# Optimization experiments

Measured on AMD Instinct MI355X. Metric: run time of the kernel, lower is better.

Reference implementation:

```python
import jax, jax.numpy as jnp
import numpy as np

NEG_SLOPE = 0.01


def reference(feat_src, feat_dst, src, dst, attn_l, attn_r):
    # feat_src: [Ns, D], feat_dst: [Nd, D], src/dst: [E] int, attn_*: [1, D]
    n_dst = feat_dst.shape[0]
    el = (feat_src * attn_l).sum(axis=-1)  # [Ns]
    er = (feat_dst * attn_r).sum(axis=-1)  # [Nd]
    e = el[src] + er[dst]                  # [E]
    e = jnp.where(e >= 0, e, NEG_SLOPE * e)  # leaky_relu
    # edge softmax over incoming edges of each destination node
    m = jax.ops.segment_max(e, dst, num_segments=n_dst)  # [Nd]
    m = jnp.where(jnp.isfinite(m), m, 0.0)  # guard empty segments
    a = jnp.exp(e - m[dst])                 # [E]
    denom = jax.ops.segment_sum(a, dst, num_segments=n_dst)  # [Nd]
    denom = jnp.where(denom > 0, denom, 1.0)
    a = a / denom[dst]
    # weighted scatter-sum of source features: [E, D] messages -> [Nd, D]
    msg = feat_src[src] * a[:, None]
    out = jax.ops.segment_sum(msg, dst, num_segments=n_dst)
    return out


def setup_inputs() -> dict:
    key = jax.random.key(0)
    k1, k2, k3, k4, k5, k6 = jax.random.split(key, 6)
    Ns, Nd, E, D = 100000, 100000, 1600000, 128
    return {
        "feat_src": jax.random.normal(k1, (Ns, D), dtype=jnp.float32),
        "feat_dst": jax.random.normal(k2, (Nd, D), dtype=jnp.float32),
        "src": jax.random.randint(k3, (E,), 0, Ns, dtype=jnp.int32),
        "dst": jax.random.randint(k4, (E,), 0, Nd, dtype=jnp.int32),
        "attn_l": jax.random.normal(k5, (1, D), dtype=jnp.float32) * 0.1,
        "attn_r": jax.random.normal(k6, (1, D), dtype=jnp.float32) * 0.1,
    }
```

## Files before the change

### kernel.cpp

```cpp
#include <hip/hip_runtime.h>
#include <hip/hip_bf16.h>
#include <math.h>

#define D 128
#define AGG_THREADS 128
#define CHUNK 512
#define BSHIFT 8
#define MAXB 1024
#define MAXWG 1024
#define PCHUNK 4096
#define PE 16
#define EBUF_CAP 5120
#define PR 8192

__device__ __forceinline__ unsigned short f2bf(float f) {
    union { float f; unsigned int u; } c; c.f = f;
    unsigned int u = c.u;
    unsigned int r = (u + 0x7FFFu + ((u >> 16) & 1u)) >> 16;
    return (unsigned short)r;
}
__device__ __forceinline__ void unpack2(unsigned int w, float& lo, float& hi) {
    union { unsigned int u; float f; } c;
    c.u = w << 16;          lo = c.f;
    c.u = w & 0xFFFF0000u;  hi = c.f;
}

__global__ void prep_kernel(const float* __restrict__ feat_src,
                            const float* __restrict__ feat_dst,
                            const float* __restrict__ attn_l,
                            const float* __restrict__ attn_r,
                            float* __restrict__ el, float* __restrict__ er,
                            unsigned short* __restrict__ feat_bf, int store_bf,
                            int Ns, int Nd) {
    int half = threadIdx.x >> 5;
    int lane = threadIdx.x & 31;
    int node = blockIdx.x * 8 + half;
    if (node >= Ns + Nd) return;
    bool is_src = node < Ns;
    const float* feat = is_src ? feat_src + (size_t)node * D
                               : feat_dst + (size_t)(node - Ns) * D;
    const float* attn = is_src ? attn_l : attn_r;
    float4 a = ((const float4*)attn)[lane];
    float4 v = ((const float4*)feat)[lane];
    if (is_src && store_bf) {
        ushort4 h; h.x = f2bf(v.x); h.y = f2bf(v.y); h.z = f2bf(v.z); h.w = f2bf(v.w);
        ((ushort4*)(feat_bf + (size_t)node * D))[lane] = h;
    }
    float s = v.x * a.x + v.y * a.y + v.z * a.z + v.w * a.w;
    #pragma unroll
    for (int off = 16; off > 0; off >>= 1)
        s += __shfl_xor(s, off, 64);
    if (lane == 0) {
        if (is_src) el[node] = s;
        else        er[node - Ns] = s;
    }
}

__global__ void partition_kernel(const int* __restrict__ src, const int* __restrict__ dst,
                                 int E, int nbk,
                                 uint2* __restrict__ bins,
                                 int* __restrict__ cnt_tab, int* __restrict__ loc_tab) {
    __shared__ int hist[MAXB];
    __shared__ int lstart[MAXB];
    __shared__ int cursor[MAXB];
    __shared__ uint2 sbuf[PCHUNK];
    int w = blockIdx.x, tid = threadIdx.x;
    int e0 = w * PCHUNK;
    int e1 = min(E, e0 + PCHUNK);
    int n = e1 - e0;

    for (int i = tid; i < nbk; i += 256) hist[i] = 0;
    __syncthreads();

    int es[PE], ed[PE];
    #pragma unroll
    for (int k = 0; k < PE; ++k) {
        int idx = e0 + k * 256 + tid;
        if (idx < e1) {
            es[k] = src[idx];
            ed[k] = dst[idx];
            atomicAdd(&hist[ed[k] >> BSHIFT], 1);
        }
    }
    __syncthreads();

    if (tid < 64) {
        int carry = 0;
        for (int c = 0; c < nbk; c += 64) {
            int i = c + tid;
            int v = (i < nbk) ? hist[i] : 0;
            int x = v;
            #pragma unroll
            for (int off = 1; off < 64; off <<= 1) {
                int t = __shfl_up(x, off, 64);
                if (tid >= off) x += t;
            }
            if (i < nbk) lstart[i] = x - v + carry;
            carry += __shfl(x, 63, 64);
        }
    }
    __syncthreads();

    for (int i = tid; i < nbk; i += 256) {
        cnt_tab[(size_t)w * nbk + i] = hist[i];
        loc_tab[(size_t)w * nbk + i] = lstart[i];
        cursor[i] = 0;
    }
    __syncthreads();

    #pragma unroll
    for (int k = 0; k < PE; ++k) {
        int idx = e0 + k * 256 + tid;
        if (idx < e1) {
            int b = ed[k] >> BSHIFT;
            int r = lstart[b] + atomicAdd(&cursor[b], 1);
            sbuf[r] = make_uint2((unsigned)es[k], (unsigned)ed[k]);
        }
    }
    __syncthreads();

    uint2* obase = bins + (size_t)w * PCHUNK;
    for (int t = tid; t < n; t += 256) obase[t] = sbuf[t];
}

__global__ void bucket_kernel(const uint2* __restrict__ bins,
                              const int* __restrict__ cnt_tab, const int* __restrict__ loc_tab,
                              int nbk, int nwg,
                              int* __restrict__ counts, int* __restrict__ offs,
                              int* __restrict__ perm, int Nd) {
    __shared__ uint2 ebuf[EBUF_CAP];
    __shared__ int wcnt[MAXWG];
    __shared__ int wdst[MAXWG];
    __shared__ int sbase[MAXWG];
    __shared__ int cnt256[256];
    __shared__ int off256[256];
    __shared__ int cur256[256];
    __shared__ int tile[256];
    __shared__ int total_sh;

    int b = blockIdx.x, tid = threadIdx.x;
    int base = b << BSHIFT;

    for (int i = tid; i < nwg; i += 256) wcnt[i] = cnt_tab[(size_t)i * nbk + b];
    __syncthreads();
    if (tid < 64) {
        int carry = 0;
        for (int c = 0; c < nwg; c += 64) {
            int i = c + tid;
            int v = (i < nwg) ? wcnt[i] : 0;
            int x = v;
            #pragma unroll
            for (int off = 1; off < 64; off <<= 1) {
                int t = __shfl_up(x, off, 64);
                if (tid >= off) x += t;
            }
            if (i < nwg) wdst[i] = x - v + carry;
            carry += __shfl(x, 63, 64);
        }
        if (tid == 0) total_sh = carry;
    }
    cnt256[tid] = 0;
    cur256[tid] = 0;
    __syncthreads();
    int n = total_sh;
    bool fits = (n <= EBUF_CAP);

    if (fits) {
        for (int w = tid; w < nwg; w += 256)
            sbase[w] = w * PCHUNK + loc_tab[(size_t)w * nbk + b] - wdst[w];
        __syncthreads();
        for (int t = tid; t < n; t += 256) {
            int lo = 0, hi = nwg - 1;
            while (lo < hi) {
                int mid = (lo + hi + 1) >> 1;
                if (wdst[mid] <= t) lo = mid; else hi = mid - 1;
            }
            uint2 e = bins[(size_t)(sbase[lo] + t)];
            ebuf[t] = e;
            atomicAdd(&cnt256[(int)e.y - base], 1);
        }
    } else {
        for (int w = tid; w < nwg; w += 256) {
            int c = wcnt[w];
            const uint2* sp = bins + (size_t)w * PCHUNK + loc_tab[(size_t)w * nbk + b];
            for (int k = 0; k < c; ++k)
                atomicAdd(&cnt256[(int)sp[k].y - base], 1);
        }
        __syncthreads();
    }
    __syncthreads();

    int v = cnt256[tid];
    tile[tid] = v;
    __syncthreads();
    for (int off = 1; off < 256; off <<= 1) {
        int t = (tid >= off) ? tile[tid - off] : 0;
        __syncthreads();
        tile[tid] += t;
        __syncthreads();
    }
    int myoff = tile[tid] - v;
    off256[tid] = myoff;
    int i = base + tid;
    if (i < Nd) {
        int c = v;
        if (myoff + c > PR) c = max(0, PR - myoff);
        counts[i] = c;
        offs[i]   = myoff;
    }
    __syncthreads();

    size_t rbase = (size_t)b * PR;
    if (fits) {
        for (int t = tid; t < n; t += 256) {
            uint2 e = ebuf[t];
            int d = (int)e.y - base;
            int r = atomicAdd(&cur256[d], 1);
            int slot = off256[d] + r;
            if (slot < PR) perm[rbase + slot] = (int)e.x;
        }
    } else {
        for (int w = tid; w < nwg; w += 256) {
            int c = wcnt[w];
            const uint2* sp = bins + (size_t)w * PCHUNK + loc_tab[(size_t)w * nbk + b];
            for (int k = 0; k < c; ++k) {
                uint2 e = sp[k];
                int d = (int)e.y - base;
                int r = atomicAdd(&cur256[d], 1);
                int slot = off256[d] + r;
                if (slot < PR) perm[rbase + slot] = (int)e.x;
            }
        }
    }
}

__device__ __forceinline__ float block_max128(float v, float* red, int tid) {
    #pragma unroll
    for (int off = 32; off > 0; off >>= 1)
        v = fmaxf(v, __shfl_down(v, off, 64));
    __syncthreads();
    if ((tid & 63) == 0) red[tid >> 6] = v;
    __syncthreads();
    return fmaxf(red[0], red[1]);
}
__device__ __forceinline__ float block_sum128(float v, float* red, int tid) {
    #pragma unroll
    for (int off = 32; off > 0; off >>= 1)
        v += __shfl_down(v, off, 64);
    __syncthreads();
    if ((tid & 63) == 0) red[tid >> 6] = v;
    __syncthreads();
    return red[0] + red[1];
}

__global__ void gat_aggregate_wave_kernel(const unsigned short* __restrict__ feat_bf,
                                          const float* __restrict__ el,
                                          const float* __restrict__ er,
                                          const int* __restrict__ offs,
                                          const int* __restrict__ counts,
                                          const int* __restrict__ perm,
                                          float* __restrict__ out, int Nd) {
    int wid  = threadIdx.x >> 6;
    int lane = threadIdx.x & 63;
    int j = blockIdx.x * 4 + wid;
    if (j >= Nd) return;
    int cnt = counts[j];
    size_t orow = (size_t)j * D;
    if (cnt == 0) {
        ((float2*)(out + orow))[lane] = make_float2(0.0f, 0.0f);
        return;
    }
    size_t beg = (size_t)(j >> BSHIFT) * PR + (size_t)offs[j];
    float erj = er[j];
    int sg = lane >> 4, u = lane & 15;
    const unsigned short* fb = feat_bf + (size_t)u * 8;
    float acc[8];
    #pragma unroll
    for (int k = 0; k < 8; ++k) acc[k] = 0.0f;

    if (cnt <= 64) {
        int s = 0; float e = -INFINITY;
        if (lane < cnt) {
            s = perm[beg + lane];
            float t = el[s] + erj;
            e = (t >= 0.0f) ? t : 0.01f * t;
        }
        float m = e;
        #pragma unroll
        for (int off = 32; off > 0; off >>= 1)
            m = fmaxf(m, __shfl_xor(m, off, 64));
        float a = (lane < cnt) ? __expf(e - m) : 0.0f;
        float den = a;
        #pragma unroll
        for (int off = 32; off > 0; off >>= 1)
            den += __shfl_xor(den, off, 64);
        a *= (1.0f / den);
        int nit = (cnt + 3) >> 2;
        for (int it = 0; it < nit; ++it) {
            int t = sg + (it << 2);
            int tt = (t < cnt) ? t : 0;
            float w = __shfl(a, tt, 64);
            int st  = __shfl(s, tt, 64);
            if (t < cnt) {
                uint4 v = *(const uint4*)(fb + (size_t)st * D);
                float f[8];
                unpack2(v.x, f[0], f[1]); unpack2(v.y, f[2], f[3]);
                unpack2(v.z, f[4], f[5]); unpack2(v.w, f[6], f[7]);
                #pragma unroll
                for (int k = 0; k < 8; ++k) acc[k] += w * f[k];
            }
        }
    } else {
        float lmax = -INFINITY;
        for (int t = lane; t < cnt; t += 64) {
            int s = perm[beg + t];
            float e = el[s] + erj;
            e = (e >= 0.0f) ? e : 0.01f * e;
            lmax = fmaxf(lmax, e);
        }
        float m = lmax;
        #pragma unroll
        for (int off = 32; off > 0; off >>= 1)
            m = fmaxf(m, __shfl_xor(m, off, 64));
        float lsum = 0.0f;
        for (int t = lane; t < cnt; t += 64) {
            int s = perm[beg + t];
            float e = el[s] + erj;
            e = (e >= 0.0f) ? e : 0.01f * e;
            lsum += __expf(e - m);
        }
        #pragma unroll
        for (int off = 32; off > 0; off >>= 1)
            lsum += __shfl_xor(lsum, off, 64);
        float inv = 1.0f / lsum;
        for (int bb = 0; bb < cnt; bb += 64) {
            int nn = min(64, cnt - bb);
            int s = 0; float a = 0.0f;
            if (lane < nn) {
                s = perm[beg + bb + lane];
                float e = el[s] + erj;
                e = (e >= 0.0f) ? e : 0.01f * e;
                a = __expf(e - m) * inv;
            }
            int nit = (nn + 3) >> 2;
            for (int it = 0; it < nit; ++it) {
                int t = sg + (it << 2);
                int tt = (t < nn) ? t : 0;
                float w = __shfl(a, tt, 64);
                int st  = __shfl(s, tt, 64);
                if (t < nn) {
                    uint4 v = *(const uint4*)(fb + (size_t)st * D);
                    float f[8];
                    unpack2(v.x, f[0], f[1]); unpack2(v.y, f[2], f[3]);
                    unpack2(v.z, f[4], f[5]); unpack2(v.w, f[6], f[7]);
                    #pragma unroll
                    for (int k = 0; k < 8; ++k) acc[k] += w * f[k];
                }
            }
        }
    }
    #pragma unroll
    for (int k = 0; k < 8; ++k) {
        acc[k] += __shfl_xor(acc[k], 16, 64);
        acc[k] += __shfl_xor(acc[k], 32, 64);
    }
    if (sg == 0) {
        float* op = out + orow + (size_t)u * 8;
        ((float4*)op)[0] = make_float4(acc[0], acc[1], acc[2], acc[3]);
        ((float4*)op)[1] = make_float4(acc[4], acc[5], acc[6], acc[7]);
    }
}

__global__ void hist_kernel(const int* __restrict__ dst, int E, int* __restrict__ counts) {
    int stride = gridDim.x * blockDim.x;
    for (int k = blockIdx.x * blockDim.x + threadIdx.x; k < E; k += stride)
        atomicAdd(&counts[dst[k]], 1);
}
__global__ void scan1_kernel(const int* __restrict__ counts, int* __restrict__ offsets,
                             int* __restrict__ blockSums, int N) {
    __shared__ int tile[256];
    int tid = threadIdx.x;
    int i = blockIdx.x * 256 + tid;
    int v = (i < N) ? counts[i] : 0;
    tile[tid] = v;
    __syncthreads();
    for (int off = 1; off < 256; off <<= 1) {
        int t = (tid >= off) ? tile[tid - off] : 0;
        __syncthreads();
        tile[tid] += t;
        __syncthreads();
    }
    int incl = tile[tid];
    if (i < N) offsets[i] = incl - v;
    if (tid == 255) blockSums[blockIdx.x] = incl;
}
__global__ void scan2_kernel(int* __restrict__ bs, int nb) {
    __shared__ int tile[256];
    int tid = threadIdx.x;
    int carry = 0;
    for (int base = 0; base < nb; base += 256) {
        int i = base + tid;
        int v = (i < nb) ? bs[i] : 0;
        __syncthreads();
        tile[tid] = v;
        __syncthreads();
        for (int off = 1; off < 256; off <<= 1) {
            int t = (tid >= off) ? tile[tid - off] : 0;
            __syncthreads();
            tile[tid] += t;
            __syncthreads();
        }
        int incl = tile[tid];
        if (i < nb) bs[i] = incl - v + carry;
        carry += tile[255];
    }
}
__global__ void fill_kernel(const int* __restrict__ src, const int* __restrict__ dst, int E,
                            const int* __restrict__ offsets, const int* __restrict__ bsum,
                            int* __restrict__ cursor, int* __restrict__ perm_src) {
    int stride = gridDim.x * blockDim.x;
    for (int k = blockIdx.x * blockDim.x + threadIdx.x; k < E; k += stride) {
        int j = dst[k];
        int p = offsets[j] + bsum[j >> BSHIFT] + atomicAdd(&cursor[j], 1);
        perm_src[p] = src[k];
    }
}
__global__ void gat_aggregate_f32_kernel(const float* __restrict__ feat_src,
                                         const float* __restrict__ el,
                                         const float* __restrict__ er,
                                         const int* __restrict__ offsets,
                                         const int* __restrict__ bsum,
                                         const int* __restrict__ counts,
                                         const int* __restrict__ perm_src,
                                         float* __restrict__ out, int Nd) {
    __shared__ float w_sh[CHUNK];
    __shared__ int   s_sh[CHUNK];
    __shared__ float red[2];
    int j = blockIdx.x;
    int tid = threadIdx.x;
    int cnt = counts[j];
    size_t orow = (size_t)j * D;
    if (cnt == 0) { out[orow + tid] = 0.0f; return; }
    int beg = offsets[j] + bsum[j >> BSHIFT];
    float erj = er[j];
    float acc = 0.0f;
    float inv;
    if (cnt <= CHUNK) {
        float lmax = -INFINITY;
        for (int t = tid; t < cnt; t += AGG_THREADS) {
            int s = perm_src[beg + t];
            float e = el[s] + erj;
            e = (e >= 0.0f) ? e : 0.01f * e;
            s_sh[t] = s; w_sh[t] = e;
            lmax = fmaxf(lmax, e);
        }
        float m = block_max128(lmax, red, tid);
        float lsum = 0.0f;
        for (int t = tid; t < cnt; t += AGG_THREADS) {
            float a = __expf(w_sh[t] - m);
            w_sh[t] = a; lsum += a;
        }
        float den = block_sum128(lsum, red, tid);
        inv = 1.0f / den;
        __syncthreads();
        for (int t = 0; t < cnt; ++t)
            acc += feat_src[(size_t)s_sh[t] * D + tid] * w_sh[t];
    } else {
        float lmax = -INFINITY;
        for (int t = tid; t < cnt; t += AGG_THREADS) {
            int s = perm_src[beg + t];
            float e = el[s] + erj;
            e = (e >= 0.0f) ? e : 0.01f * e;
            lmax = fmaxf(lmax, e);
        }
        float m = block_max128(lmax, red, tid);
        float lsum = 0.0f;
        for (int t = tid; t < cnt; t += AGG_THREADS) {
            int s = perm_src[beg + t];
            float e = el[s] + erj;
            e = (e >= 0.0f) ? e : 0.01f * e;
            lsum += __expf(e - m);
        }
        float den = block_sum128(lsum, red, tid);
        inv = 1.0f / den;
        for (int bb = 0; bb < cnt; bb += CHUNK) {
            int n = min(CHUNK, cnt - bb);
            __syncthreads();
            for (int t = tid; t < n; t += AGG_THREADS) {
                int s = perm_src[beg + bb + t];
                float e = el[s] + erj;
                e = (e >= 0.0f) ? e : 0.01f * e;
                s_sh[t] = s;
                w_sh[t] = __expf(e - m);
            }
            __syncthreads();
            for (int t = 0; t < n; ++t)
                acc += feat_src[(size_t)s_sh[t] * D + tid] * w_sh[t];
        }
    }
    out[orow + tid] = acc * inv;
}

extern "C" void kernel_launch(void* const* d_in, const int* in_sizes, int n_in,
                              void* d_out, int out_size, void* d_ws, size_t ws_size,
                              hipStream_t stream) {
    const float* feat_src = (const float*)d_in[0];
    const float* feat_dst = (const float*)d_in[1];
    const int*   src      = (const int*)d_in[2];
    const int*   dst      = (const int*)d_in[3];
    const float* attn_l   = (const float*)d_in[4];
    const float* attn_r   = (const float*)d_in[5];
    float* out = (float*)d_out;

    int Ns = in_sizes[0] / D;
    int Nd = in_sizes[1] / D;
    int E  = in_sizes[2];
    int NBK = (Nd + (1 << BSHIFT) - 1) >> BSHIFT;
    int NWG = (E + PCHUNK - 1) / PCHUNK;

    char* p = (char*)d_ws;
    auto carve = [&](size_t bytes) { void* r = (void*)p; p += (bytes + 255) & ~(size_t)255; return r; };
    float* el      = (float*)carve((size_t)Ns * 4);
    float* er      = (float*)carve((size_t)Nd * 4);
    int*   counts  = (int*)carve((size_t)Nd * 4);
    int*   offs    = (int*)carve((size_t)Nd * 4);
    int*   gcursor = (int*)carve((size_t)Nd * 4);
    int*   bsums   = (int*)carve((size_t)NBK * 4);
    int*   cnt_tab = (int*)carve((size_t)NWG * NBK * 4);
    int*   loc_tab = (int*)carve((size_t)NWG * NBK * 4);
    int*   perm    = (int*)carve((size_t)NBK * PR * 4);
    uint2* bins    = (uint2*)carve((size_t)NWG * PCHUNK * 8);
    size_t used    = (size_t)(p - (char*)d_ws);
    size_t bf_bytes = (size_t)Ns * D * 2;
    unsigned short* feat_bf = (unsigned short*)carve(bf_bytes);

    int fast = (NBK <= MAXB && NWG <= MAXWG &&
                used + bf_bytes + 256 <= ws_size) ? 1 : 0;

    int total = Ns + Nd;
    if (fast) {
        prep_kernel<<<(total + 7) / 8, 256, 0, stream>>>(feat_src, feat_dst, attn_l, attn_r,
                                                         el, er, feat_bf, 1, Ns, Nd);
        partition_kernel<<<NWG, 256, 0, stream>>>(src, dst, E, NBK, bins, cnt_tab, loc_tab);
        bucket_kernel<<<NBK, 256, 0, stream>>>(bins, cnt_tab, loc_tab, NBK, NWG,
                                               counts, offs, perm, Nd);
        gat_aggregate_wave_kernel<<<(Nd + 3) / 4, 256, 0, stream>>>(feat_bf, el, er, offs,
                                                                    counts, perm, out, Nd);
    } else {
        hipMemsetAsync(counts, 0, (size_t)Nd * 4, stream);
        hipMemsetAsync(gcursor, 0, (size_t)Nd * 4, stream);
        prep_kernel<<<(total + 7) / 8, 256, 0, stream>>>(feat_src, feat_dst, attn_l, attn_r,
                                                         el, er, nullptr, 0, Ns, Nd);
        hist_kernel<<<2048, 256, 0, stream>>>(dst, E, counts);
        scan1_kernel<<<NBK, 256, 0, stream>>>(counts, offs, bsums, Nd);
        scan2_kernel<<<1, 256, 0, stream>>>(bsums, NBK);
        fill_kernel<<<2048, 256, 0, stream>>>(src, dst, E, offs, bsums, gcursor, perm);
        gat_aggregate_f32_kernel<<<Nd, AGG_THREADS, 0, stream>>>(feat_src, el, er, offs,
                                                                 bsums, counts, perm, out, Nd);
    }
}
```

Baseline: 265.1 us.

## Replace two-pass bucketed partition with atomic histogram, scan and fill CSR build

Removes the partition and bucket kernels that built a per-bucket, capped-size edge permutation. The destination histogram is now folded into the prep kernel as a grid-stride atomic loop, followed by a global two-level scan and an atomic fill kernel that produces an exact CSR permutation. The aggregation kernel now indexes it through offsets plus block sums. This drops the per-bucket PR cap and the intermediate bins buffer. In exchange it relies on global atomics with random scatter in the fill step, adds more launches and memsets, and loses the locality of the bucketed layout.

```diff
diff --git a/kernel.cpp b/kernel.cpp
--- a/kernel.cpp
+++ b/kernel.cpp
@@ -6,12 +6,6 @@
 #define AGG_THREADS 128
 #define CHUNK 512
 #define BSHIFT 8
-#define MAXB 1024
-#define MAXWG 1024
-#define PCHUNK 4096
-#define PE 16
-#define EBUF_CAP 5120
-#define PR 8192
 
 __device__ __forceinline__ unsigned short f2bf(float f) {
     union { float f; unsigned int u; } c; c.f = f;
@@ -29,9 +23,16 @@
                             const float* __restrict__ feat_dst,
                             const float* __restrict__ attn_l,
                             const float* __restrict__ attn_r,
+                            const int* __restrict__ dst, int E,
+                            int* __restrict__ counts,
                             float* __restrict__ el, float* __restrict__ er,
                             unsigned short* __restrict__ feat_bf, int store_bf,
                             int Ns, int Nd) {
+    int gid = blockIdx.x * 256 + threadIdx.x;
+    int gstride = gridDim.x * 256;
+    for (int k = gid; k < E; k += gstride)
+        atomicAdd(&counts[dst[k]], 1);
+
     int half = threadIdx.x >> 5;
     int lane = threadIdx.x & 31;
     int node = blockIdx.x * 8 + half;
@@ -56,141 +57,12 @@
     }
 }
 
-__global__ void partition_kernel(const int* __restrict__ src, const int* __restrict__ dst,
-                                 int E, int nbk,
-                                 uint2* __restrict__ bins,
-                                 int* __restrict__ cnt_tab, int* __restrict__ loc_tab) {
-    __shared__ int hist[MAXB];
-    __shared__ int lstart[MAXB];
-    __shared__ int cursor[MAXB];
-    __shared__ uint2 sbuf[PCHUNK];
-    int w = blockIdx.x, tid = threadIdx.x;
-    int e0 = w * PCHUNK;
-    int e1 = min(E, e0 + PCHUNK);
-    int n = e1 - e0;
-
-    for (int i = tid; i < nbk; i += 256) hist[i] = 0;
-    __syncthreads();
-
-    int es[PE], ed[PE];
-    #pragma unroll
-    for (int k = 0; k < PE; ++k) {
-        int idx = e0 + k * 256 + tid;
-        if (idx < e1) {
-            es[k] = src[idx];
-            ed[k] = dst[idx];
-            atomicAdd(&hist[ed[k] >> BSHIFT], 1);
-        }
-    }
-    __syncthreads();
-
-    if (tid < 64) {
-        int carry = 0;
-        for (int c = 0; c < nbk; c += 64) {
-            int i = c + tid;
-            int v = (i < nbk) ? hist[i] : 0;
-            int x = v;
-            #pragma unroll
-            for (int off = 1; off < 64; off <<= 1) {
-                int t = __shfl_up(x, off, 64);
-                if (tid >= off) x += t;
-            }
-            if (i < nbk) lstart[i] = x - v + carry;
-            carry += __shfl(x, 63, 64);
-        }
-    }
-    __syncthreads();
-
-    for (int i = tid; i < nbk; i += 256) {
-        cnt_tab[(size_t)w * nbk + i] = hist[i];
-        loc_tab[(size_t)w * nbk + i] = lstart[i];
-        cursor[i] = 0;
-    }
-    __syncthreads();
-
-    #pragma unroll
-    for (int k = 0; k < PE; ++k) {
-        int idx = e0 + k * 256 + tid;
-        if (idx < e1) {
-            int b = ed[k] >> BSHIFT;
-            int r = lstart[b] + atomicAdd(&cursor[b], 1);
-            sbuf[r] = make_uint2((unsigned)es[k], (unsigned)ed[k]);
-        }
-    }
-    __syncthreads();
-
-    uint2* obase = bins + (size_t)w * PCHUNK;
-    for (int t = tid; t < n; t += 256) obase[t] = sbuf[t];
-}
-
-__global__ void bucket_kernel(const uint2* __restrict__ bins,
-                              const int* __restrict__ cnt_tab, const int* __restrict__ loc_tab,
-                              int nbk, int nwg,
-                              int* __restrict__ counts, int* __restrict__ offs,
-                              int* __restrict__ perm, int Nd) {
-    __shared__ uint2 ebuf[EBUF_CAP];
-    __shared__ int wcnt[MAXWG];
-    __shared__ int wdst[MAXWG];
-    __shared__ int sbase[MAXWG];
-    __shared__ int cnt256[256];
-    __shared__ int off256[256];
-    __shared__ int cur256[256];
+__global__ void scan1_kernel(const int* __restrict__ counts, int* __restrict__ offsets,
+                             int* __restrict__ blockSums, int N) {
     __shared__ int tile[256];
-    __shared__ int total_sh;
-
-    int b = blockIdx.x, tid = threadIdx.x;
-    int base = b << BSHIFT;
-
-    for (int i = tid; i < nwg; i += 256) wcnt[i] = cnt_tab[(size_t)i * nbk + b];
-    __syncthreads();
-    if (tid < 64) {
-        int carry = 0;
-        for (int c = 0; c < nwg; c += 64) {
-            int i = c + tid;
-            int v = (i < nwg) ? wcnt[i] : 0;
-            int x = v;
-            #pragma unroll
-            for (int off = 1; off < 64; off <<= 1) {
-                int t = __shfl_up(x, off, 64);
-                if (tid >= off) x += t;
-            }
-            if (i < nwg) wdst[i] = x - v + carry;
-            carry += __shfl(x, 63, 64);
-        }
-        if (tid == 0) total_sh = carry;
-    }
-    cnt256[tid] = 0;
-    cur256[tid] = 0;
-    __syncthreads();
-    int n = total_sh;
-    bool fits = (n <= EBUF_CAP);
-
-    if (fits) {
-        for (int w = tid; w < nwg; w += 256)
-            sbase[w] = w * PCHUNK + loc_tab[(size_t)w * nbk + b] - wdst[w];
-        __syncthreads();
-        for (int t = tid; t < n; t += 256) {
-            int lo = 0, hi = nwg - 1;
-            while (lo < hi) {
-                int mid = (lo + hi + 1) >> 1;
-                if (wdst[mid] <= t) lo = mid; else hi = mid - 1;
-            }
-            uint2 e = bins[(size_t)(sbase[lo] + t)];
-            ebuf[t] = e;
-            atomicAdd(&cnt256[(int)e.y - base], 1);
-        }
-    } else {
-        for (int w = tid; w < nwg; w += 256) {
-            int c = wcnt[w];
-            const uint2* sp = bins + (size_t)w * PCHUNK + loc_tab[(size_t)w * nbk + b];
-            for (int k = 0; k < c; ++k)
-                atomicAdd(&cnt256[(int)sp[k].y - base], 1);
-        }
-        __syncthreads();
-    }
-    __syncthreads();
-
-    int v = cnt256[tid];
+    int tid = threadIdx.x;
+    int i = blockIdx.x * 256 + tid;
+    int v = (i < N) ? counts[i] : 0;
     tile[tid] = v;
     __syncthreads();
     for (int off = 1; off < 256; off <<= 1) {
@@ -199,38 +71,40 @@
         tile[tid] += t;
         __syncthreads();
     }
-    int myoff = tile[tid] - v;
-    off256[tid] = myoff;
-    int i = base + tid;
-    if (i < Nd) {
-        int c = v;
-        if (myoff + c > PR) c = max(0, PR - myoff);
-        counts[i] = c;
-        offs[i]   = myoff;
-    }
-    __syncthreads();
-
-    size_t rbase = (size_t)b * PR;
-    if (fits) {
-        for (int t = tid; t < n; t += 256) {
-            uint2 e = ebuf[t];
-            int d = (int)e.y - base;
-            int r = atomicAdd(&cur256[d], 1);
-            int slot = off256[d] + r;
-            if (slot < PR) perm[rbase + slot] = (int)e.x;
-        }
-    } else {
-        for (int w = tid; w < nwg; w += 256) {
-            int c = wcnt[w];
-            const uint2* sp = bins + (size_t)w * PCHUNK + loc_tab[(size_t)w * nbk + b];
-            for (int k = 0; k < c; ++k) {
-                uint2 e = sp[k];
-                int d = (int)e.y - base;
-                int r = atomicAdd(&cur256[d], 1);
-                int slot = off256[d] + r;
-                if (slot < PR) perm[rbase + slot] = (int)e.x;
-            }
-        }
+    int incl = tile[tid];
+    if (i < N) offsets[i] = incl - v;
+    if (tid == 255) blockSums[blockIdx.x] = incl;
+}
+__global__ void scan2_kernel(int* __restrict__ bs, int nb) {
+    __shared__ int tile[256];
+    int tid = threadIdx.x;
+    int carry = 0;
+    for (int base = 0; base < nb; base += 256) {
+        int i = base + tid;
+        int v = (i < nb) ? bs[i] : 0;
+        __syncthreads();
+        tile[tid] = v;
+        __syncthreads();
+        for (int off = 1; off < 256; off <<= 1) {
+            int t = (tid >= off) ? tile[tid - off] : 0;
+            __syncthreads();
+            tile[tid] += t;
+            __syncthreads();
+        }
+        int incl = tile[tid];
+        if (i < nb) bs[i] = incl - v + carry;
+        carry += tile[255];
+    }
+}
+
+__global__ void fill_kernel(const int* __restrict__ src, const int* __restrict__ dst, int E,
+                            const int* __restrict__ offsets, const int* __restrict__ bsum,
+                            int* __restrict__ cursor, int* __restrict__ perm_src) {
+    int stride = gridDim.x * blockDim.x;
+    for (int k = blockIdx.x * blockDim.x + threadIdx.x; k < E; k += stride) {
+        int j = dst[k];
+        int p = offsets[j] + bsum[j >> BSHIFT] + atomicAdd(&cursor[j], 1);
+        perm_src[p] = src[k];
     }
 }
 
@@ -257,6 +131,7 @@
                                           const float* __restrict__ el,
                                           const float* __restrict__ er,
                                           const int* __restrict__ offs,
+                                          const int* __restrict__ bsum,
                                           const int* __restrict__ counts,
                                           const int* __restrict__ perm,
                                           float* __restrict__ out, int Nd) {
@@ -270,7 +145,7 @@
         ((float2*)(out + orow))[lane] = make_float2(0.0f, 0.0f);
         return;
     }
-    size_t beg = (size_t)(j >> BSHIFT) * PR + (size_t)offs[j];
+    size_t beg = (size_t)offs[j] + (size_t)bsum[j >> BSHIFT];
     float erj = er[j];
     int sg = lane >> 4, u = lane & 15;
     const unsigned short* fb = feat_bf + (size_t)u * 8;
@@ -371,60 +246,6 @@
     }
 }
 
-__global__ void hist_kernel(const int* __restrict__ dst, int E, int* __restrict__ counts) {
-    int stride = gridDim.x * blockDim.x;
-    for (int k = blockIdx.x * blockDim.x + threadIdx.x; k < E; k += stride)
-        atomicAdd(&counts[dst[k]], 1);
-}
-__global__ void scan1_kernel(const int* __restrict__ counts, int* __restrict__ offsets,
-                             int* __restrict__ blockSums, int N) {
-    __shared__ int tile[256];
-    int tid = threadIdx.x;
-    int i = blockIdx.x * 256 + tid;
-    int v = (i < N) ? counts[i] : 0;
-    tile[tid] = v;
-    __syncthreads();
-    for (int off = 1; off < 256; off <<= 1) {
-        int t = (tid >= off) ? tile[tid - off] : 0;
-        __syncthreads();
-        tile[tid] += t;
-        __syncthreads();
-    }
-    int incl = tile[tid];
-    if (i < N) offsets[i] = incl - v;
-    if (tid == 255) blockSums[blockIdx.x] = incl;
-}
-__global__ void scan2_kernel(int* __restrict__ bs, int nb) {
-    __shared__ int tile[256];
-    int tid = threadIdx.x;
-    int carry = 0;
-    for (int base = 0; base < nb; base += 256) {
-        int i = base + tid;
-        int v = (i < nb) ? bs[i] : 0;
-        __syncthreads();
-        tile[tid] = v;
-        __syncthreads();
-        for (int off = 1; off < 256; off <<= 1) {
-            int t = (tid >= off) ? tile[tid - off] : 0;
-            __syncthreads();
-            tile[tid] += t;
-            __syncthreads();
-        }
-        int incl = tile[tid];
-        if (i < nb) bs[i] = incl - v + carry;
-        carry += tile[255];
-    }
-}
-__global__ void fill_kernel(const int* __restrict__ src, const int* __restrict__ dst, int E,
-                            const int* __restrict__ offsets, const int* __restrict__ bsum,
-                            int* __restrict__ cursor, int* __restrict__ perm_src) {
-    int stride = gridDim.x * blockDim.x;
-    for (int k = blockIdx.x * blockDim.x + threadIdx.x; k < E; k += stride) {
-        int j = dst[k];
-        int p = offsets[j] + bsum[j >> BSHIFT] + atomicAdd(&cursor[j], 1);
-        perm_src[p] = src[k];
-    }
-}
 __global__ void gat_aggregate_f32_kernel(const float* __restrict__ feat_src,
                                          const float* __restrict__ el,
                                          const float* __restrict__ er,
@@ -516,7 +337,6 @@
     int Nd = in_sizes[1] / D;
     int E  = in_sizes[2];
     int NBK = (Nd + (1 << BSHIFT) - 1) >> BSHIFT;
-    int NWG = (E + PCHUNK - 1) / PCHUNK;
 
     char* p = (char*)d_ws;
     auto carve = [&](size_t bytes) { void* r = (void*)p; p += (bytes + 255) & ~(size_t)255; return r; };
@@ -526,35 +346,29 @@
     int*   offs    = (int*)carve((size_t)Nd * 4);
     int*   gcursor = (int*)carve((size_t)Nd * 4);
     int*   bsums   = (int*)carve((size_t)NBK * 4);
-    int*   cnt_tab = (int*)carve((size_t)NWG * NBK * 4);
-    int*   loc_tab = (int*)carve((size_t)NWG * NBK * 4);
-    int*   perm    = (int*)carve((size_t)NBK * PR * 4);
-    uint2* bins    = (uint2*)carve((size_t)NWG * PCHUNK * 8);
+    int*   perm    = (int*)carve((size_t)E * 4);
     size_t used    = (size_t)(p - (char*)d_ws);
     size_t bf_bytes = (size_t)Ns * D * 2;
     unsigned short* feat_bf = (unsigned short*)carve(bf_bytes);
 
-    int fast = (NBK <= MAXB && NWG <= MAXWG &&
-                used + bf_bytes + 256 <= ws_size) ? 1 : 0;
+    int use_bf = (used + bf_bytes + 256 <= ws_size) ? 1 : 0;
+
+    hipMemsetAsync(counts, 0, (size_t)Nd * 4, stream);
+    hipMemsetAsync(gcursor, 0, (size_t)Nd * 4, stream);
 
     int total = Ns + Nd;
-    if (fast) {
-        prep_kernel<<<(total + 7) / 8, 256, 0, stream>>>(feat_src, feat_dst, attn_l, attn_r,
-                                                         el, er, feat_bf, 1, Ns, Nd);
-        partition_kernel<<<NWG, 256, 0, stream>>>(src, dst, E, NBK, bins, cnt_tab, loc_tab);
-        bucket_kernel<<<NBK, 256, 0, stream>>>(bins, cnt_tab, loc_tab, NBK, NWG,
-                                               counts, offs, perm, Nd);
+    int pgrid = (total + 7) / 8;
+    if (pgrid < 1024) pgrid = 1024;
+    prep_kernel<<<pgrid, 256, 0, stream>>>(feat_src, feat_dst, attn_l, attn_r,
+                                           dst, E, counts,
+                                           el, er, feat_bf, use_bf, Ns, Nd);
+    scan1_kernel<<<NBK, 256, 0, stream>>>(counts, offs, bsums, Nd);
+    scan2_kernel<<<1, 256, 0, stream>>>(bsums, NBK);
+    fill_kernel<<<2048, 256, 0, stream>>>(src, dst, E, offs, bsums, gcursor, perm);
+    if (use_bf) {
         gat_aggregate_wave_kernel<<<(Nd + 3) / 4, 256, 0, stream>>>(feat_bf, el, er, offs,
-                                                                    counts, perm, out, Nd);
+                                                                    bsums, counts, perm, out, Nd);
     } else {
-        hipMemsetAsync(counts, 0, (size_t)Nd * 4, stream);
-        hipMemsetAsync(gcursor, 0, (size_t)Nd * 4, stream);
-        prep_kernel<<<(total + 7) / 8, 256, 0, stream>>>(feat_src, feat_dst, attn_l, attn_r,
-                                                         el, er, nullptr, 0, Ns, Nd);
-        hist_kernel<<<2048, 256, 0, stream>>>(dst, E, counts);
-        scan1_kernel<<<NBK, 256, 0, stream>>>(counts, offs, bsums, Nd);
-        scan2_kernel<<<1, 256, 0, stream>>>(bsums, NBK);
-        fill_kernel<<<2048, 256, 0, stream>>>(src, dst, E, offs, bsums, gcursor, perm);
         gat_aggregate_f32_kernel<<<Nd, AGG_THREADS, 0, stream>>>(feat_src, el, er, offs,
                                                                  bsums, counts, perm, out, Nd);
     }
```

Result: slower. 377.6 us (+42.4%).
